# Kernel optimization log

Hardware: AMD Instinct MI355X
Metric: run time of the kernel (lower is better)

The kernel has to match this reference:

```python
import jax, jax.numpy as jnp
import numpy as np

H = 8  # head_count


def setup_inputs() -> dict:
    key = jax.random.key(0)
    ks = jax.random.split(key, 9)
    n, C, w = 8, 512, 8192
    Kc, Vc = 512, 512
    s = 0.02
    return {
        "x": jax.random.normal(ks[0], (n, C, w), dtype=jnp.float32),
        "Wk": jax.random.normal(ks[1], (Kc, C), dtype=jnp.float32) * s,
        "bk": jax.random.normal(ks[2], (Kc,), dtype=jnp.float32) * s,
        "Wq": jax.random.normal(ks[3], (Kc, C), dtype=jnp.float32) * s,
        "bq": jax.random.normal(ks[4], (Kc,), dtype=jnp.float32) * s,
        "Wv": jax.random.normal(ks[5], (Vc, C), dtype=jnp.float32) * s,
        "bv": jax.random.normal(ks[6], (Vc,), dtype=jnp.float32) * s,
        "Wr": jax.random.normal(ks[7], (C, Vc), dtype=jnp.float32) * s,
        "br": jax.random.normal(ks[8], (C,), dtype=jnp.float32) * s,
    }


def reference(x, Wk, bk, Wq, bq, Wv, bv, Wr, br):
    n, C, w = x.shape
    Kc, Vc = Wk.shape[0], Wv.shape[0]
    hk, hv = Kc // H, Vc // H
    # 1x1 Conv1d == channel-mixing GEMM
    keys = jnp.einsum('kc,ncw->nkw', Wk, x) + bk[None, :, None]
    queries = jnp.einsum('kc,ncw->nkw', Wq, x) + bq[None, :, None]
    values = jnp.einsum('vc,ncw->nvw', Wv, x) + bv[None, :, None]
    # split heads: [n, H, hd, w]
    K = jax.nn.softmax(keys.reshape(n, H, hk, w), axis=-1)   # softmax over positions
    Q = jax.nn.softmax(queries.reshape(n, H, hk, w), axis=2)  # softmax over channels
    V = values.reshape(n, H, hv, w)
    # context = K @ V^T : [n, H, hk, hv]
    ctx = jnp.einsum('nhkw,nhvw->nhkv', K, V)
    # attended = ctx^T @ Q : [n, H, hv, w]
    att = jnp.einsum('nhkv,nhkw->nhvw', ctx, Q).reshape(n, Vc, w)
    out = jnp.einsum('cv,nvw->ncw', Wr, att) + br[None, :, None] + x
    return out
```

## Files before the change

### kernel.cpp

```cpp
#include <hip/hip_runtime.h>
#include <hip/hip_bf16.h>
#include <cstdint>

#define NB 8
#define CD 512
#define WD 8192
#define NH 8

typedef __bf16 bf16x8 __attribute__((ext_vector_type(8)));
typedef float  f32x4  __attribute__((ext_vector_type(4)));
typedef float  f32x16 __attribute__((ext_vector_type(16)));

__device__ __forceinline__ void gload_lds16(const __bf16* g, __bf16* l) {
  __builtin_amdgcn_global_load_lds((const __attribute__((address_space(1))) void*)g,
                                   (__attribute__((address_space(3))) void*)l,
                                   16, 0, 0);
}

__global__ void __launch_bounds__(256) prep_x_kernel(const float* __restrict__ x,
                                                     __bf16* __restrict__ xT) {
  __shared__ float tile[64][65];
  const int n = blockIdx.z, cb = blockIdx.y * 64, wb = blockIdx.x * 64;
  const int t = threadIdx.x;
  const int lr = t >> 4;
  const int lw4 = (t & 15) * 4;
  const float* xp = x + ((size_t)n * CD + cb) * WD + wb;
#pragma unroll
  for (int it = 0; it < 4; it++) {
    const int cc = it * 16 + lr;
    const f32x4 v = *(const f32x4*)(xp + (size_t)cc * WD + lw4);
    tile[cc][lw4 + 0] = v[0];
    tile[cc][lw4 + 1] = v[1];
    tile[cc][lw4 + 2] = v[2];
    tile[cc][lw4 + 3] = v[3];
  }
  __syncthreads();
  const int c8 = (t & 7) * 8;
  __bf16* op = xT + ((size_t)n * WD + wb) * CD + cb;
#pragma unroll
  for (int it = 0; it < 2; it++) {
    const int ww = it * 32 + (t >> 3);
    bf16x8 o;
#pragma unroll
    for (int e = 0; e < 8; e++) o[e] = (__bf16)tile[c8 + e][ww];
    *(bf16x8*)(op + (size_t)ww * CD + c8) = o;
  }
}

__global__ void __launch_bounds__(256) prep_w_kernel(const float* __restrict__ Wk,
                                                     const float* __restrict__ Wq,
                                                     const float* __restrict__ Wv,
                                                     const float* __restrict__ Wr,
                                                     const float* __restrict__ bk,
                                                     const float* __restrict__ bv,
                                                     __bf16* __restrict__ WkvB,
                                                     __bf16* __restrict__ WqB,
                                                     __bf16* __restrict__ WrB,
                                                     float* __restrict__ bkv) {
  const int gid = blockIdx.x * 256 + threadIdx.x;
  WkvB[gid]          = (__bf16)Wk[gid];
  WkvB[262144 + gid] = (__bf16)Wv[gid];
  WqB[gid]           = (__bf16)Wq[gid];
  WrB[gid]           = (__bf16)Wr[gid];
  if (gid < 512)       bkv[gid] = bk[gid];
  else if (gid < 1024) bkv[gid] = bv[gid - 512];
}

#define STAGE_SLAB(Ak, Bk, lds, t)                                          \
  _Pragma("unroll") for (int rnd = 0; rnd < 8; rnd++) {                     \
    const int c = rnd * 256 + (t);                                          \
    const int cc = c & 1023;                                                \
    const int r = cc >> 3;                                                  \
    const int g = (cc & 7) ^ (r & 7);                                       \
    const __bf16* src = ((c >> 10) ? (Bk) : (Ak)) + (size_t)r * 512 + g * 8;\
    gload_lds16(src, (lds) + (size_t)c * 8);                                \
  }

__device__ __forceinline__ void gemm_lds_core(const __bf16* __restrict__ A,
                                              const __bf16* __restrict__ B,
                                              f32x4 (&acc)[4][4], __bf16* lds) {
  const int t = threadIdx.x;
  const int lane = t & 63, wave = t >> 6;
  const int l15 = lane & 15, quad = lane >> 4;
  const int wm = (wave >> 1) << 6, wn = (wave & 1) << 6;
#pragma unroll 1
  for (int kc = 0; kc < 8; kc++) {
    const __bf16* Ak = A + kc * 64;
    const __bf16* Bk = B + kc * 64;
    STAGE_SLAB(Ak, Bk, lds, t)
    __syncthreads();
#pragma unroll
    for (int k0 = 0; k0 < 2; k0++) {
      const int gk = k0 * 4 + quad;
      bf16x8 av[4], bv[4];
#pragma unroll
      for (int i = 0; i < 4; i++) {
        const int r = wm + i * 16 + l15;
        av[i] = *(const bf16x8*)(lds + (size_t)((r << 3) + (gk ^ (r & 7))) * 8);
      }
#pragma unroll
      for (int j = 0; j < 4; j++) {
        const int r = wn + j * 16 + l15;
        bv[j] = *(const bf16x8*)(lds + (size_t)(8192 + (r << 3) + (gk ^ (r & 7))) * 8);
      }
#pragma unroll
      for (int i = 0; i < 4; i++)
#pragma unroll
        for (int j = 0; j < 4; j++)
          acc[i][j] = __builtin_amdgcn_mfma_f32_16x16x32_bf16(av[i], bv[j], acc[i][j], 0, 0, 0);
    }
    __syncthreads();
  }
}

__device__ __forceinline__ void gemm_lds_core32(const __bf16* __restrict__ A,
                                                const __bf16* __restrict__ B,
                                                f32x16 (&acc)[2][2], __bf16* lds) {
  const int t = threadIdx.x;
  const int lane = t & 63, wave = t >> 6;
  const int l31 = lane & 31, khalf = lane >> 5;
  const int wm = (wave >> 1) << 6, wn = (wave & 1) << 6;
#pragma unroll 1
  for (int kc = 0; kc < 8; kc++) {
    const __bf16* Ak = A + kc * 64;
    const __bf16* Bk = B + kc * 64;
    STAGE_SLAB(Ak, Bk, lds, t)
    __syncthreads();
#pragma unroll
    for (int kk = 0; kk < 4; kk++) {
      const int g = kk * 2 + khalf;
      bf16x8 av[2], bv[2];
#pragma unroll
      for (int i = 0; i < 2; i++) {
        const int r = wm + i * 32 + l31;
        av[i] = *(const bf16x8*)(lds + (size_t)((r << 3) + (g ^ (r & 7))) * 8);
      }
#pragma unroll
      for (int j = 0; j < 2; j++) {
        const int r = wn + j * 32 + l31;
        bv[j] = *(const bf16x8*)(lds + (size_t)(8192 + (r << 3) + (g ^ (r & 7))) * 8);
      }
#pragma unroll
      for (int i = 0; i < 2; i++)
#pragma unroll
        for (int j = 0; j < 2; j++)
          acc[i][j] = __builtin_amdgcn_mfma_f32_32x32x16_bf16(av[i], bv[j], acc[i][j], 0, 0, 0);
    }
    __syncthreads();
  }
}

__global__ void __launch_bounds__(256) gemm_kv_kernel(const __bf16* __restrict__ WkvB,
                                                      const __bf16* __restrict__ xT,
                                                      const float* __restrict__ bkv,
                                                      __bf16* __restrict__ kv) {
  __shared__ __bf16 lds[16384];
  const int n = blockIdx.z, m0 = blockIdx.y * 128, w0 = blockIdx.x * 128;
  f32x16 acc[2][2];
#pragma unroll
  for (int i = 0; i < 2; i++)
#pragma unroll
    for (int j = 0; j < 2; j++)
#pragma unroll
      for (int r = 0; r < 16; r++) acc[i][j][r] = 0.f;
  gemm_lds_core32(WkvB + (size_t)m0 * 512, xT + ((size_t)n * WD + w0) * 512, acc, lds);
  const int t = threadIdx.x, lane = t & 63, wave = t >> 6;
  const int l31 = lane & 31, khalf = lane >> 5;
  const int wm = (wave >> 1) << 6, wn = (wave & 1) << 6;
  __bf16* outp = kv + (size_t)n * 1024 * WD + w0 + wn + l31;
#pragma unroll
  for (int i = 0; i < 2; i++)
#pragma unroll
    for (int reg = 0; reg < 16; reg++) {
      const int row = (reg & 3) + 8 * (reg >> 2) + 4 * khalf;
      const int m = m0 + wm + i * 32 + row;
      const float bias = bkv[m];
      __bf16* rp = outp + (size_t)m * WD;
#pragma unroll
      for (int j = 0; j < 2; j++) rp[j * 32] = (__bf16)(acc[i][j][reg] + bias);
    }
}

__global__ void __launch_bounds__(256) gemm_qT_kernel(const __bf16* __restrict__ xT,
                                                      const __bf16* __restrict__ WqB,
                                                      const float* __restrict__ bq,
                                                      __bf16* __restrict__ qT) {
  __shared__ __bf16 lds[16384];
  const int n = blockIdx.z, w0 = blockIdx.x * 128, q0 = blockIdx.y * 128;
  f32x4 acc[4][4];
#pragma unroll
  for (int i = 0; i < 4; i++)
#pragma unroll
    for (int j = 0; j < 4; j++) acc[i][j] = (f32x4){0.f, 0.f, 0.f, 0.f};
  gemm_lds_core(xT + ((size_t)n * WD + w0) * 512, WqB + (size_t)q0 * 512, acc, lds);
  const int t = threadIdx.x, lane = t & 63, wave = t >> 6;
  const int l15 = lane & 15, quad = lane >> 4;
  const int wm = (wave >> 1) << 6, wn = (wave & 1) << 6;
  float bqv[4];
#pragma unroll
  for (int j = 0; j < 4; j++) bqv[j] = bq[q0 + wn + j * 16 + l15];
#pragma unroll
  for (int i = 0; i < 4; i++)
#pragma unroll
    for (int r = 0; r < 4; r++) {
      float e[4];
      float s = 0.f;
#pragma unroll
      for (int j = 0; j < 4; j++) {
        e[j] = __expf(acc[i][j][r] + bqv[j]);
        s += e[j];
      }
      s += __shfl_xor(s, 1);
      s += __shfl_xor(s, 2);
      s += __shfl_xor(s, 4);
      s += __shfl_xor(s, 8);
      const float inv = 1.0f / s;
      const int w = w0 + wm + i * 16 + quad * 4 + r;
      __bf16* rp = qT + ((size_t)n * WD + w) * 512 + q0 + wn + l15;
#pragma unroll
      for (int j = 0; j < 4; j++) rp[j * 16] = (__bf16)(e[j] * inv);
    }
}

__global__ void __launch_bounds__(256) gemm_out_kernel(const __bf16* __restrict__ Mf,
                                                       const __bf16* __restrict__ qT,
                                                       const float* __restrict__ br,
                                                       const float* __restrict__ x,
                                                       float* __restrict__ out) {
  __shared__ __bf16 lds[16384];
  const int n = blockIdx.z, c0 = blockIdx.y * 128, w0 = blockIdx.x * 128;
  f32x16 acc[2][2];
#pragma unroll
  for (int i = 0; i < 2; i++)
#pragma unroll
    for (int j = 0; j < 2; j++)
#pragma unroll
      for (int r = 0; r < 16; r++) acc[i][j][r] = 0.f;
  gemm_lds_core32(Mf + ((size_t)n * 512 + c0) * 512, qT + ((size_t)n * WD + w0) * 512, acc, lds);
  const int t = threadIdx.x, lane = t & 63, wave = t >> 6;
  const int l31 = lane & 31, khalf = lane >> 5;
  const int wm = (wave >> 1) << 6, wn = (wave & 1) << 6;
#pragma unroll
  for (int i = 0; i < 2; i++)
#pragma unroll
    for (int reg = 0; reg < 16; reg++) {
      const int row = (reg & 3) + 8 * (reg >> 2) + 4 * khalf;
      const int c = c0 + wm + i * 32 + row;
      const float bias = br[c];
      const size_t base = ((size_t)n * CD + c) * WD + w0 + wn + l31;
#pragma unroll
      for (int j = 0; j < 2; j++)
        out[base + j * 32] = acc[i][j][reg] + bias + x[base + j * 32];
    }
}

__global__ void __launch_bounds__(256) ctx_kernel(const __bf16* __restrict__ kv,
                                                  float* __restrict__ partial,
                                                  float* __restrict__ ssum) {
  const int chunk = blockIdx.x, h = blockIdx.y, n = blockIdx.z;
  const int t = threadIdx.x, lane = t & 63, wave = t >> 6;
  const int l15 = lane & 15, quad = lane >> 4;
  const int krow = h * 64 + wave * 16 + l15;
  const __bf16* Kp = kv + ((size_t)n * 1024 + krow) * WD + chunk * 1024 + quad * 8;
  const __bf16* Vp = kv + ((size_t)n * 1024 + 512 + h * 64 + l15) * WD + chunk * 1024 + quad * 8;
  f32x4 acc[4];
#pragma unroll
  for (int j = 0; j < 4; j++) acc[j] = (f32x4){0.f, 0.f, 0.f, 0.f};
  float esum = 0.f;
  for (int s = 0; s < 32; s++) {
    bf16x8 kraw = *(const bf16x8*)(Kp + s * 32);
    bf16x8 af;
#pragma unroll
    for (int e = 0; e < 8; e++) {
      const float ev = __expf((float)kraw[e]);
      esum += ev;
      af[e] = (__bf16)ev;
    }
#pragma unroll
    for (int j = 0; j < 4; j++) {
      bf16x8 bv = *(const bf16x8*)(Vp + (size_t)(j * 16) * WD + s * 32);
      acc[j] = __builtin_amdgcn_mfma_f32_16x16x32_bf16(af, bv, acc[j], 0, 0, 0);
    }
  }
  esum += __shfl_xor(esum, 16);
  esum += __shfl_xor(esum, 32);
  float* pp = partial + (((size_t)(n * 8 + h) * 8 + chunk) << 12);
#pragma unroll
  for (int j = 0; j < 4; j++)
#pragma unroll
    for (int r = 0; r < 4; r++) {
      const int kr = wave * 16 + quad * 4 + r;
      const int vc = j * 16 + l15;
      pp[kr * 64 + vc] = acc[j][r];
    }
  if (lane < 16)
    ssum[(((size_t)(n * 8 + h) * 8 + chunk) << 6) + wave * 16 + l15] = esum;
}

__global__ void __launch_bounds__(256) ctx_finish_kernel(const float* __restrict__ partial,
                                                         const float* __restrict__ ssum,
                                                         const __bf16* __restrict__ WrB,
                                                         __bf16* __restrict__ Mf) {
  __shared__ __bf16 ctx_tile[64][72];
  __shared__ float srow[64];
  const int h = blockIdx.x, n = blockIdx.y;
  const int nh = n * 8 + h;
  const int t = threadIdx.x;
  if (t < 64) {
    float s = 0.f;
#pragma unroll
    for (int c = 0; c < 8; c++) s += ssum[(((size_t)nh * 8 + c) << 6) + t];
    srow[t] = 1.0f / s;
  }
  __syncthreads();
  const float* pp = partial + ((size_t)nh << 15);
#pragma unroll
  for (int i = 0; i < 16; i++) {
    const int kvi = i * 256 + t;
    float v = 0.f;
#pragma unroll
    for (int c = 0; c < 8; c++) v += pp[((size_t)c << 12) + kvi];
    ctx_tile[kvi >> 6][kvi & 63] = (__bf16)(v * srow[kvi >> 6]);
  }
  __syncthreads();
  const int lane = t & 63, wave = t >> 6;
  const int l15 = lane & 15, quad = lane >> 4;
#pragma unroll 1
  for (int ms = 0; ms < 4; ms++) {
    f32x4 acc[2][4];
#pragma unroll
    for (int i = 0; i < 2; i++)
#pragma unroll
      for (int j = 0; j < 4; j++) acc[i][j] = (f32x4){0.f, 0.f, 0.f, 0.f};
    const __bf16* Ap = WrB + (size_t)(ms * 128 + wave * 32 + l15) * 512 + h * 64 + quad * 8;
#pragma unroll
    for (int k0 = 0; k0 < 64; k0 += 32) {
      bf16x8 av[2];
#pragma unroll
      for (int i = 0; i < 2; i++) av[i] = *(const bf16x8*)(Ap + i * 16 * 512 + k0);
#pragma unroll
      for (int j = 0; j < 4; j++) {
        bf16x8 bv = *(const bf16x8*)(&ctx_tile[j * 16 + l15][quad * 8 + k0]);
#pragma unroll
        for (int i = 0; i < 2; i++)
          acc[i][j] = __builtin_amdgcn_mfma_f32_16x16x32_bf16(av[i], bv, acc[i][j], 0, 0, 0);
      }
    }
#pragma unroll
    for (int i = 0; i < 2; i++)
#pragma unroll
      for (int j = 0; j < 4; j++)
#pragma unroll
        for (int r = 0; r < 4; r++) {
          const int c = ms * 128 + wave * 32 + i * 16 + quad * 4 + r;
          const int col = h * 64 + j * 16 + l15;
          Mf[((size_t)n * 512 + c) * 512 + col] = (__bf16)acc[i][j][r];
        }
  }
}

extern "C" void kernel_launch(void* const* d_in, const int* in_sizes, int n_in,
                              void* d_out, int out_size, void* d_ws, size_t ws_size,
                              hipStream_t stream) {
  (void)in_sizes; (void)n_in; (void)out_size; (void)ws_size;
  const float* x  = (const float*)d_in[0];
  const float* Wk = (const float*)d_in[1];
  const float* bk = (const float*)d_in[2];
  const float* Wq = (const float*)d_in[3];
  const float* bq = (const float*)d_in[4];
  const float* Wv = (const float*)d_in[5];
  const float* bv = (const float*)d_in[6];
  const float* Wr = (const float*)d_in[7];
  const float* br = (const float*)d_in[8];
  float* out = (float*)d_out;

  char* ws = (char*)d_ws;
  __bf16* xT      = (__bf16*)ws;
  float*  partial = (float*)ws;
  __bf16* Mf      = (__bf16*)(ws + (20ull << 20));
  __bf16* kv      = (__bf16*)(ws + (64ull << 20));
  __bf16* qT      = (__bf16*)(ws + (192ull << 20));

  char* scr = (char*)d_out + (124ull << 20);
  __bf16* WkvB = (__bf16*)scr;
  __bf16* WqB  = (__bf16*)(scr + (1ull << 20));
  __bf16* WrB  = (__bf16*)(scr + (1536ull << 10));
  float*  bkv  = (float*)(scr + (2ull << 20));
  float*  ssum = (float*)(scr + (2ull << 20) + 65536);

  prep_x_kernel<<<dim3(128, 8, 8), 256, 0, stream>>>(x, xT);
  prep_w_kernel<<<dim3(1024), 256, 0, stream>>>(Wk, Wq, Wv, Wr, bk, bv, WkvB, WqB, WrB, bkv);
  gemm_kv_kernel<<<dim3(64, 8, 8), 256, 0, stream>>>(WkvB, xT, bkv, kv);
  gemm_qT_kernel<<<dim3(64, 4, 8), 256, 0, stream>>>(xT, WqB, bq, qT);
  ctx_kernel<<<dim3(8, 8, 8), 256, 0, stream>>>(kv, partial, ssum);
  ctx_finish_kernel<<<dim3(8, 8), 256, 0, stream>>>(partial, ssum, WrB, Mf);
  gemm_out_kernel<<<dim3(64, 4, 8), 256, 0, stream>>>(Mf, qT, br, x, out);
}
```

Measured before the change: 503.1 us.

## Fuse K/V projection with context accumulation to skip the kv intermediate

```diff
diff --git a/kernel.cpp b/kernel.cpp
--- a/kernel.cpp
+++ b/kernel.cpp
@@ -58,12 +58,19 @@
                                                      __bf16* __restrict__ WrB,
                                                      float* __restrict__ bkv) {
   const int gid = blockIdx.x * 256 + threadIdx.x;
-  WkvB[gid]          = (__bf16)Wk[gid];
-  WkvB[262144 + gid] = (__bf16)Wv[gid];
-  WqB[gid]           = (__bf16)Wq[gid];
-  WrB[gid]           = (__bf16)Wr[gid];
-  if (gid < 512)       bkv[gid] = bk[gid];
-  else if (gid < 1024) bkv[gid] = bv[gid - 512];
+  const int r = gid >> 9;
+  const int cpos = gid & 511;
+  const int h = r >> 6, wi = r & 63;
+  WkvB[((size_t)(h * 128 + wi) << 9) + cpos]      = (__bf16)Wk[gid];
+  WkvB[((size_t)(h * 128 + 64 + wi) << 9) + cpos] = (__bf16)Wv[gid];
+  WqB[gid] = (__bf16)Wq[gid];
+  WrB[gid] = (__bf16)Wr[gid];
+  if (gid < 512) {
+    bkv[(gid >> 6) * 128 + (gid & 63)] = bk[gid];
+  } else if (gid < 1024) {
+    const int rr = gid - 512;
+    bkv[(rr >> 6) * 128 + 64 + (rr & 63)] = bv[rr];
+  }
 }
 
 #define STAGE_SLAB(Ak, Bk, lds, t)                                          \
@@ -150,12 +157,14 @@
   }
 }
 
-__global__ void __launch_bounds__(256) gemm_kv_kernel(const __bf16* __restrict__ WkvB,
-                                                      const __bf16* __restrict__ xT,
-                                                      const float* __restrict__ bkv,
-                                                      __bf16* __restrict__ kv) {
-  __shared__ __bf16 lds[16384];
-  const int n = blockIdx.z, m0 = blockIdx.y * 128, w0 = blockIdx.x * 128;
+#define LDE 136
+__global__ void __launch_bounds__(256) gemm_kvctx_kernel(const __bf16* __restrict__ WkvB,
+                                                         const __bf16* __restrict__ xT,
+                                                         const float* __restrict__ bkv,
+                                                         float* __restrict__ ctx_accum,
+                                                         float* __restrict__ ssum) {
+  __shared__ __bf16 smem[2 * 64 * LDE];
+  const int n = blockIdx.z, h = blockIdx.y, w0 = blockIdx.x * 128;
   f32x16 acc[2][2];
 #pragma unroll
   for (int i = 0; i < 2; i++)
@@ -163,22 +172,62 @@
     for (int j = 0; j < 2; j++)
 #pragma unroll
       for (int r = 0; r < 16; r++) acc[i][j][r] = 0.f;
-  gemm_lds_core32(WkvB + (size_t)m0 * 512, xT + ((size_t)n * WD + w0) * 512, acc, lds);
+  gemm_lds_core32(WkvB + ((size_t)h * 128) * 512, xT + ((size_t)n * WD + w0) * 512, acc, smem);
+
   const int t = threadIdx.x, lane = t & 63, wave = t >> 6;
   const int l31 = lane & 31, khalf = lane >> 5;
-  const int wm = (wave >> 1) << 6, wn = (wave & 1) << 6;
-  __bf16* outp = kv + (size_t)n * 1024 * WD + w0 + wn + l31;
+  const int l15 = lane & 15, quad = lane >> 4;
+  const int wm = (wave >> 1) << 6, wn = (wave & 1) << 6;
+  __bf16* ek = smem;
+  __bf16* vt = smem + 64 * LDE;
+  const bool isK = (wm == 0);
 #pragma unroll
   for (int i = 0; i < 2; i++)
 #pragma unroll
     for (int reg = 0; reg < 16; reg++) {
       const int row = (reg & 3) + 8 * (reg >> 2) + 4 * khalf;
-      const int m = m0 + wm + i * 32 + row;
-      const float bias = bkv[m];
-      __bf16* rp = outp + (size_t)m * WD;
-#pragma unroll
-      for (int j = 0; j < 2; j++) rp[j * 32] = (__bf16)(acc[i][j][reg] + bias);
-    }
+      const int lr = i * 32 + row;
+      const float bias = bkv[h * 128 + wm + lr];
+#pragma unroll
+      for (int j = 0; j < 2; j++) {
+        const int w = wn + j * 32 + l31;
+        const float val = acc[i][j][reg] + bias;
+        if (isK) ek[lr * LDE + w] = (__bf16)__expf(val);
+        else     vt[lr * LDE + w] = (__bf16)val;
+      }
+    }
+  __syncthreads();
+
+  f32x4 cacc[4];
+  f32x4 sacc = (f32x4){0.f, 0.f, 0.f, 0.f};
+#pragma unroll
+  for (int jj = 0; jj < 4; jj++) cacc[jj] = (f32x4){0.f, 0.f, 0.f, 0.f};
+  bf16x8 ones;
+#pragma unroll
+  for (int e = 0; e < 8; e++) ones[e] = (__bf16)1.0f;
+#pragma unroll
+  for (int ks = 0; ks < 4; ks++) {
+    const bf16x8 av = *(const bf16x8*)(ek + (wave * 16 + l15) * LDE + ks * 32 + quad * 8);
+    sacc = __builtin_amdgcn_mfma_f32_16x16x32_bf16(av, ones, sacc, 0, 0, 0);
+#pragma unroll
+    for (int jj = 0; jj < 4; jj++) {
+      const bf16x8 bvv = *(const bf16x8*)(vt + (jj * 16 + l15) * LDE + ks * 32 + quad * 8);
+      cacc[jj] = __builtin_amdgcn_mfma_f32_16x16x32_bf16(av, bvv, cacc[jj], 0, 0, 0);
+    }
+  }
+  float* cp = ctx_accum + ((size_t)(n * 8 + h) << 12);
+#pragma unroll
+  for (int jj = 0; jj < 4; jj++)
+#pragma unroll
+    for (int r = 0; r < 4; r++) {
+      const int k = wave * 16 + quad * 4 + r;
+      atomicAdd(cp + k * 64 + jj * 16 + l15, cacc[jj][r]);
+    }
+  if (l15 == 0) {
+#pragma unroll
+    for (int r = 0; r < 4; r++)
+      atomicAdd(ssum + ((size_t)(n * 8 + h) << 6) + wave * 16 + quad * 4 + r, sacc[r]);
+  }
 }
 
 __global__ void __launch_bounds__(256) gemm_qT_kernel(const __bf16* __restrict__ xT,
@@ -254,50 +303,7 @@
     }
 }
 
-__global__ void __launch_bounds__(256) ctx_kernel(const __bf16* __restrict__ kv,
-                                                  float* __restrict__ partial,
-                                                  float* __restrict__ ssum) {
-  const int chunk = blockIdx.x, h = blockIdx.y, n = blockIdx.z;
-  const int t = threadIdx.x, lane = t & 63, wave = t >> 6;
-  const int l15 = lane & 15, quad = lane >> 4;
-  const int krow = h * 64 + wave * 16 + l15;
-  const __bf16* Kp = kv + ((size_t)n * 1024 + krow) * WD + chunk * 1024 + quad * 8;
-  const __bf16* Vp = kv + ((size_t)n * 1024 + 512 + h * 64 + l15) * WD + chunk * 1024 + quad * 8;
-  f32x4 acc[4];
-#pragma unroll
-  for (int j = 0; j < 4; j++) acc[j] = (f32x4){0.f, 0.f, 0.f, 0.f};
-  float esum = 0.f;
-  for (int s = 0; s < 32; s++) {
-    bf16x8 kraw = *(const bf16x8*)(Kp + s * 32);
-    bf16x8 af;
-#pragma unroll
-    for (int e = 0; e < 8; e++) {
-      const float ev = __expf((float)kraw[e]);
-      esum += ev;
-      af[e] = (__bf16)ev;
-    }
-#pragma unroll
-    for (int j = 0; j < 4; j++) {
-      bf16x8 bv = *(const bf16x8*)(Vp + (size_t)(j * 16) * WD + s * 32);
-      acc[j] = __builtin_amdgcn_mfma_f32_16x16x32_bf16(af, bv, acc[j], 0, 0, 0);
-    }
-  }
-  esum += __shfl_xor(esum, 16);
-  esum += __shfl_xor(esum, 32);
-  float* pp = partial + (((size_t)(n * 8 + h) * 8 + chunk) << 12);
-#pragma unroll
-  for (int j = 0; j < 4; j++)
-#pragma unroll
-    for (int r = 0; r < 4; r++) {
-      const int kr = wave * 16 + quad * 4 + r;
-      const int vc = j * 16 + l15;
-      pp[kr * 64 + vc] = acc[j][r];
-    }
-  if (lane < 16)
-    ssum[(((size_t)(n * 8 + h) * 8 + chunk) << 6) + wave * 16 + l15] = esum;
-}
-
-__global__ void __launch_bounds__(256) ctx_finish_kernel(const float* __restrict__ partial,
+__global__ void __launch_bounds__(256) ctx_finish_kernel(const float* __restrict__ ctx_accum,
                                                          const float* __restrict__ ssum,
                                                          const __bf16* __restrict__ WrB,
                                                          __bf16* __restrict__ Mf) {
@@ -306,21 +312,13 @@
   const int h = blockIdx.x, n = blockIdx.y;
   const int nh = n * 8 + h;
   const int t = threadIdx.x;
-  if (t < 64) {
-    float s = 0.f;
-#pragma unroll
-    for (int c = 0; c < 8; c++) s += ssum[(((size_t)nh * 8 + c) << 6) + t];
-    srow[t] = 1.0f / s;
-  }
+  if (t < 64) srow[t] = 1.0f / ssum[((size_t)nh << 6) + t];
   __syncthreads();
-  const float* pp = partial + ((size_t)nh << 15);
+  const float* cp = ctx_accum + ((size_t)nh << 12);
 #pragma unroll
   for (int i = 0; i < 16; i++) {
     const int kvi = i * 256 + t;
-    float v = 0.f;
-#pragma unroll
-    for (int c = 0; c < 8; c++) v += pp[((size_t)c << 12) + kvi];
-    ctx_tile[kvi >> 6][kvi & 63] = (__bf16)(v * srow[kvi >> 6]);
+    ctx_tile[kvi >> 6][kvi & 63] = (__bf16)(cp[kvi] * srow[kvi >> 6]);
   }
   __syncthreads();
   const int lane = t & 63, wave = t >> 6;
@@ -375,24 +373,23 @@
   float* out = (float*)d_out;
 
   char* ws = (char*)d_ws;
-  __bf16* xT      = (__bf16*)ws;
-  float*  partial = (float*)ws;
-  __bf16* Mf      = (__bf16*)(ws + (20ull << 20));
-  __bf16* kv      = (__bf16*)(ws + (64ull << 20));
-  __bf16* qT      = (__bf16*)(ws + (192ull << 20));
+  __bf16* xT = (__bf16*)ws;
+  __bf16* Mf = (__bf16*)(ws + (64ull << 20));
+  __bf16* qT = (__bf16*)(ws + (192ull << 20));
 
   char* scr = (char*)d_out + (124ull << 20);
-  __bf16* WkvB = (__bf16*)scr;
-  __bf16* WqB  = (__bf16*)(scr + (1ull << 20));
-  __bf16* WrB  = (__bf16*)(scr + (1536ull << 10));
-  float*  bkv  = (float*)(scr + (2ull << 20));
-  float*  ssum = (float*)(scr + (2ull << 20) + 65536);
+  __bf16* WkvB     = (__bf16*)scr;
+  __bf16* WqB      = (__bf16*)(scr + (1ull << 20));
+  __bf16* WrB      = (__bf16*)(scr + (1536ull << 10));
+  float*  bkv      = (float*)(scr + (2ull << 20));
+  float*  ctx_accum = (float*)(scr + (2560ull << 10));
+  float*  ssum     = (float*)(scr + (3584ull << 10));
 
   prep_x_kernel<<<dim3(128, 8, 8), 256, 0, stream>>>(x, xT);
   prep_w_kernel<<<dim3(1024), 256, 0, stream>>>(Wk, Wq, Wv, Wr, bk, bv, WkvB, WqB, WrB, bkv);
-  gemm_kv_kernel<<<dim3(64, 8, 8), 256, 0, stream>>>(WkvB, xT, bkv, kv);
+  hipMemsetAsync(ctx_accum, 0, (1ull << 20) + (16ull << 10), stream);
+  gemm_kvctx_kernel<<<dim3(64, 8, 8), 256, 0, stream>>>(WkvB, xT, bkv, ctx_accum, ssum);
   gemm_qT_kernel<<<dim3(64, 4, 8), 256, 0, stream>>>(xT, WqB, bq, qT);
-  ctx_kernel<<<dim3(8, 8, 8), 256, 0, stream>>>(kv, partial, ssum);
-  ctx_finish_kernel<<<dim3(8, 8), 256, 0, stream>>>(partial, ssum, WrB, Mf);
+  ctx_finish_kernel<<<dim3(8, 8), 256, 0, stream>>>(ctx_accum, ssum, WrB, Mf);
   gemm_out_kernel<<<dim3(64, 4, 8), 256, 0, stream>>>(Mf, qT, br, x, out);
 }
```

After: 481.2 us. 1.05x faster.
